# Performance work log

Hardware: AMD Instinct MI355X
Metric: run time of the kernel (lower is better)

The kernel has to match this reference:

```python
import jax, jax.numpy as jnp
import numpy as np

B, L, D, T = 32, 512, 1024, 256
MAX_MENTION_LEN = 10
NEG_INF = float('-inf')


def _static_bounds_and_keep():
    # Full (start, end) grid, flattened row-major like torch's .view(-1, 2)
    s = np.repeat(np.arange(L), L)
    e = np.tile(np.arange(L), L)
    bounds = np.stack([s, e], axis=-1)            # [L*L, 2]
    keep = (e - s) <= MAX_MENTION_LEN             # static per-position mask
    idx = np.nonzero(keep)[0]
    return jnp.asarray(bounds[keep], jnp.int32), jnp.asarray(idx, jnp.int32)


def setup_inputs() -> dict:
    key = jax.random.key(0)
    k0, k1, k2 = jax.random.split(key, 3)
    text_encodings = jax.random.normal(k0, (B, L, D), dtype=jnp.float32)
    mask_ctxt = jnp.ones((B, L), dtype=jnp.int32)
    # word -> wordpiece mapping: [start, end_exclusive); values kept in [1, L)
    tokens_mapping = jax.random.randint(k1, (B, T, 2), 1, L).astype(jnp.int32)
    W = jax.random.normal(k2, (D, 3), dtype=jnp.float32) * 0.02
    b = jnp.zeros((3,), dtype=jnp.float32)
    return {"text_encodings": text_encodings, "mask_ctxt": mask_ctxt,
            "tokens_mapping": tokens_mapping, "W": W, "b": b}


def reference(text_encodings, mask_ctxt, tokens_mapping, W, b):
    # per-token start / end / mention logits
    logits = jnp.einsum('bld,dk->blk', text_encodings, W) + b  # [B, L, 3]
    valid_tok = (mask_ctxt == 1)
    start_lp = jnp.where(valid_tok, logits[:, :, 0], NEG_INF)
    end_lp = jnp.where(valid_tok, logits[:, :, 1], NEG_INF)
    mention_lp = jnp.where(valid_tok, logits[:, :, 2], NEG_INF)

    # scores[b, s, e] = start[b, s] + end[b, e] + sum_{i=s..e} mention[b, i]
    scores = start_lp[:, :, None] + end_lp[:, None, :]          # [B, L, L]
    csum = jnp.cumsum(mention_lp, axis=1)                        # [B, L]
    csum_prev = jnp.concatenate(
        [jnp.zeros((csum.shape[0], 1), csum.dtype), csum[:, :-1]], axis=1)
    scores = scores + (csum[:, None, :] - csum_prev[:, :, None])

    # mention_sizes > 0  <=>  e >= s
    pos = jnp.arange(L)
    size_ok = pos[None, :, None] <= pos[None, None, :]           # [1, L, L]

    # token-boundary masks (scatter 1 at word starts / ends, zero col 0)
    bidx = jnp.arange(tokens_mapping.shape[0])[:, None]
    ts = jnp.zeros(mask_ctxt.shape, jnp.int32).at[bidx, tokens_mapping[:, :, 0]].set(1)
    ts = ts.at[:, 0].set(0)
    te = jnp.zeros(mask_ctxt.shape, jnp.int32).at[bidx, tokens_mapping[:, :, 1] - 1].set(1)
    te = te.at[:, 0].set(0)
    vse = ts[:, :, None] * te[:, None, :]                        # bmm outer product

    valid = size_ok & (mask_ctxt[:, :, None] > 0) & (vse > 0)
    scores = jnp.where(valid, scores, NEG_INF)

    scores_flat = scores.reshape(scores.shape[0], -1)            # [B, L*L]
    bounds_keep, keep_idx = _static_bounds_and_keep()
    out_scores = scores_flat[:, keep_idx]                        # [B, K]
    out_bounds = jnp.broadcast_to(bounds_keep[None],
                                  (scores.shape[0],) + bounds_keep.shape)
    return out_scores, out_bounds
```

## Files before the change

kernel.cpp:

```cpp
#include <hip/hip_runtime.h>
#include <math.h>

#define BB 32
#define LL 512
#define DD 1024
#define TT 256
#define NK 136393
#define NK_LIN 131273
#define S_LIN 502
#define NEG_BIG  -3.0e38f
#define NEG_MASK -1.0e30f
#define P_TOT (BB * NK)
#define SC4 (P_TOT / 4)
#define GEMV_BLOCKS 4096
#define MEMSET_BLOCKS ((SC4 + 255) / 256)
#define BCHUNKS ((NK + 255) / 256)
#define BGROUPS 2
#define BOUNDS_BLOCKS (BCHUNKS * BGROUPS)
#define PERIOD 9
#define QMAX 1066
#define MEGA_BLOCKS (PERIOD * QMAX)

typedef float f4v __attribute__((ext_vector_type(4)));
typedef float f2v __attribute__((ext_vector_type(2)));

__device__ __forceinline__ int off_s(int s) {
    return (s <= S_LIN) ? s * (s + 21) / 2 : NK_LIN + (s - S_LIN) * LL;
}

__global__ __launch_bounds__(256) void mega_kernel(
    const float* __restrict__ text, const float* __restrict__ W,
    const float* __restrict__ bias, const int* __restrict__ mask,
    float* __restrict__ out,
    float* __restrict__ slp, float* __restrict__ elp, float* __restrict__ mlp)
{
    const int id = blockIdx.x;
    const int q  = id / PERIOD;
    const int r  = id - q * PERIOD;

    if (r < 4) {
        const int g = q * 4 + r;
        if (g >= GEMV_BLOCKS) return;
        const int wid  = threadIdx.x >> 6;
        const int lane = threadIdx.x & 63;
        const int row  = g * 4 + wid;
        const f4v* t4 = (const f4v*)(text + (size_t)row * DD);
        const f4v* w4 = (const f4v*)W;
        float a0 = 0.f, a1 = 0.f, a2 = 0.f;
#pragma unroll
        for (int j = 0; j < 4; ++j) {
            const int fi = lane + j * 64;
            f4v v  = t4[fi];
            f4v w0 = w4[fi * 3 + 0];
            f4v w1 = w4[fi * 3 + 1];
            f4v w2 = w4[fi * 3 + 2];
            a0 += v.x * w0.x;  a1 += v.x * w0.y;  a2 += v.x * w0.z;
            a0 += v.y * w0.w;  a1 += v.y * w1.x;  a2 += v.y * w1.y;
            a0 += v.z * w1.z;  a1 += v.z * w1.w;  a2 += v.z * w2.x;
            a0 += v.w * w2.y;  a1 += v.w * w2.z;  a2 += v.w * w2.w;
        }
#pragma unroll
        for (int o = 32; o; o >>= 1) {
            a0 += __shfl_down(a0, o);
            a1 += __shfl_down(a1, o);
            a2 += __shfl_down(a2, o);
        }
        if (lane == 0) {
            const int m = mask[row];
            slp[row] = (m == 1) ? a0 + bias[0] : NEG_MASK;
            elp[row] = (m == 1) ? a1 + bias[1] : NEG_MASK;
            mlp[row] = (m == 1) ? a2 + bias[2] : NEG_MASK;
        }
        return;
    }

    if (r < 8) {
        const int m = q * 4 + (r - 4);
        if (m >= MEMSET_BLOCKS) return;
        const int i = m * 256 + threadIdx.x;
        if (i < SC4) {
            f4v neg = {NEG_BIG, NEG_BIG, NEG_BIG, NEG_BIG};
            ((f4v*)out)[i] = neg;
        }
        return;
    }

    if (q >= BOUNDS_BLOCKS) return;
    const int c = q % BCHUNKS;
    const int g = q / BCHUNKS;
    const int p = c * 256 + threadIdx.x;
    if (p >= NK) return;
    int s, e;
    if (p >= NK_LIN) {
        const int rr = p - NK_LIN;
        s = S_LIN + (rr >> 9);
        e = rr & 511;
    } else {
        float f = sqrtf(8.0f * (float)p + 441.0f);
        s = (int)((f - 21.0f) * 0.5f);
        if (s < 0) s = 0;
        if (s > 501) s = 501;
        while ((s + 1) * (s + 22) / 2 <= p) ++s;
        while (s * (s + 21) / 2 > p) --s;
        e = p - s * (s + 21) / 2;
    }
    f2v v = {(float)s, (float)e};
    f2v* bp = (f2v*)(out + (size_t)P_TOT);
#pragma unroll
    for (int j = 0; j < 16; ++j) {
        const int b = g * 16 + j;
        bp[(size_t)b * NK + p] = v;
    }
}

__global__ __launch_bounds__(512) void scatter_kernel(
    const float* __restrict__ slp, const float* __restrict__ elp,
    const float* __restrict__ mlp, const int* __restrict__ mask,
    const int* __restrict__ tmap, float* __restrict__ out)
{
    const int b = blockIdx.x;
    const int t = threadIdx.x;
    __shared__ float sl[LL], el[LL], ml[LL];
    __shared__ unsigned char tsl[LL], tel[LL];

    tsl[t] = 0; tel[t] = 0;
    const int idx = b * LL + t;
    sl[t] = slp[idx]; el[t] = elp[idx]; ml[t] = mlp[idx];
    __syncthreads();
    if (t < TT) {
        int s0 = tmap[((size_t)b * TT + t) * 2 + 0];
        int e0 = tmap[((size_t)b * TT + t) * 2 + 1] - 1;
        s0 = min(max(s0, 0), LL - 1);
        e0 = min(max(e0, 0), LL - 1);
        tsl[s0] = 1;
        tel[e0] = 1;
    }
    __syncthreads();

    const int s = t;
    if (s > 0 && tsl[s] && mask[idx] == 1) {
        const size_t obase = (size_t)b * NK + off_s(s);
        const float sv = sl[s];
        const int emax = min(LL - 1, s + 10);
        float w = 0.f;
        for (int e = s; e <= emax; ++e) {
            w += ml[e];
            if (tel[e]) {
                float sc = sv + el[e] + w;
                if (sc < -1.0e29f) sc = NEG_BIG;
                out[obase + e] = sc;
            }
        }
    }
}

extern "C" void kernel_launch(void* const* d_in, const int* in_sizes, int n_in,
                              void* d_out, int out_size, void* d_ws, size_t ws_size,
                              hipStream_t stream) {
    const float* text = (const float*)d_in[0];
    const int*   mask = (const int*)d_in[1];
    const int*   tmap = (const int*)d_in[2];
    const float* W    = (const float*)d_in[3];
    const float* bias = (const float*)d_in[4];
    float* out = (float*)d_out;

    float* slp = (float*)d_ws;
    float* elp = slp + (size_t)BB * LL;
    float* mlp = elp + (size_t)BB * LL;

    mega_kernel<<<MEGA_BLOCKS, 256, 0, stream>>>(text, W, bias, mask, out,
                                                 slp, elp, mlp);
    scatter_kernel<<<BB, 512, 0, stream>>>(slp, elp, mlp, mask, tmap, out);
}
```

Baseline: 28.53 us.

## Split fused mega kernel into separate fill, GEMV and parallel scatter kernels

Replaces the single interleaved mega kernel with a write kernel (fill and bounds), a separate GEMV kernel, and a scatter kernel launched over a 2D grid so each block handles one span length. Splitting the scatter across 11 times more blocks spreads the per-batch tail work over more CUs. The cost is an extra kernel launch, redundant shared-memory setup in every tail block, and the loss of the overlap between GEMV and memset that the interleaved block schedule provided.

```diff
diff --git a/kernel.cpp b/kernel.cpp
--- a/kernel.cpp
+++ b/kernel.cpp
@@ -12,14 +12,10 @@
 #define NEG_MASK -1.0e30f
 #define P_TOT (BB * NK)
 #define SC4 (P_TOT / 4)
-#define GEMV_BLOCKS 4096
 #define MEMSET_BLOCKS ((SC4 + 255) / 256)
 #define BCHUNKS ((NK + 255) / 256)
-#define BGROUPS 2
-#define BOUNDS_BLOCKS (BCHUNKS * BGROUPS)
-#define PERIOD 9
-#define QMAX 1066
-#define MEGA_BLOCKS (PERIOD * QMAX)
+#define D1_BLOCKS (MEMSET_BLOCKS + 2 * BCHUNKS)
+#define GEMV_BLOCKS (BB * LL / 4)
 
 typedef float f4v __attribute__((ext_vector_type(4)));
 typedef float f2v __attribute__((ext_vector_type(2)));
@@ -28,56 +24,13 @@
     return (s <= S_LIN) ? s * (s + 21) / 2 : NK_LIN + (s - S_LIN) * LL;
 }
 
-__global__ __launch_bounds__(256) void mega_kernel(
-    const float* __restrict__ text, const float* __restrict__ W,
-    const float* __restrict__ bias, const int* __restrict__ mask,
-    float* __restrict__ out,
-    float* __restrict__ slp, float* __restrict__ elp, float* __restrict__ mlp)
+__global__ __launch_bounds__(256) void write_kernel(float* __restrict__ out)
 {
     const int id = blockIdx.x;
-    const int q  = id / PERIOD;
-    const int r  = id - q * PERIOD;
+    const int t  = threadIdx.x;
 
-    if (r < 4) {
-        const int g = q * 4 + r;
-        if (g >= GEMV_BLOCKS) return;
-        const int wid  = threadIdx.x >> 6;
-        const int lane = threadIdx.x & 63;
-        const int row  = g * 4 + wid;
-        const f4v* t4 = (const f4v*)(text + (size_t)row * DD);
-        const f4v* w4 = (const f4v*)W;
-        float a0 = 0.f, a1 = 0.f, a2 = 0.f;
-#pragma unroll
-        for (int j = 0; j < 4; ++j) {
-            const int fi = lane + j * 64;
-            f4v v  = t4[fi];
-            f4v w0 = w4[fi * 3 + 0];
-            f4v w1 = w4[fi * 3 + 1];
-            f4v w2 = w4[fi * 3 + 2];
-            a0 += v.x * w0.x;  a1 += v.x * w0.y;  a2 += v.x * w0.z;
-            a0 += v.y * w0.w;  a1 += v.y * w1.x;  a2 += v.y * w1.y;
-            a0 += v.z * w1.z;  a1 += v.z * w1.w;  a2 += v.z * w2.x;
-            a0 += v.w * w2.y;  a1 += v.w * w2.z;  a2 += v.w * w2.w;
-        }
-#pragma unroll
-        for (int o = 32; o; o >>= 1) {
-            a0 += __shfl_down(a0, o);
-            a1 += __shfl_down(a1, o);
-            a2 += __shfl_down(a2, o);
-        }
-        if (lane == 0) {
-            const int m = mask[row];
-            slp[row] = (m == 1) ? a0 + bias[0] : NEG_MASK;
-            elp[row] = (m == 1) ? a1 + bias[1] : NEG_MASK;
-            mlp[row] = (m == 1) ? a2 + bias[2] : NEG_MASK;
-        }
-        return;
-    }
-
-    if (r < 8) {
-        const int m = q * 4 + (r - 4);
-        if (m >= MEMSET_BLOCKS) return;
-        const int i = m * 256 + threadIdx.x;
+    if (id < MEMSET_BLOCKS) {
+        const int i = id * 256 + t;
         if (i < SC4) {
             f4v neg = {NEG_BIG, NEG_BIG, NEG_BIG, NEG_BIG};
             ((f4v*)out)[i] = neg;
@@ -85,10 +38,10 @@
         return;
     }
 
-    if (q >= BOUNDS_BLOCKS) return;
-    const int c = q % BCHUNKS;
-    const int g = q / BCHUNKS;
-    const int p = c * 256 + threadIdx.x;
+    const int q = id - MEMSET_BLOCKS;
+    const int g = (q >= BCHUNKS) ? 1 : 0;
+    const int c = q - g * BCHUNKS;
+    const int p = c * 256 + t;
     if (p >= NK) return;
     int s, e;
     if (p >= NK_LIN) {
@@ -113,18 +66,56 @@
     }
 }
 
-__global__ __launch_bounds__(512) void scatter_kernel(
+__global__ __launch_bounds__(256) void gemv_kernel(
+    const float* __restrict__ text, const float* __restrict__ W,
+    const float* __restrict__ bias, const int* __restrict__ mask,
+    float* __restrict__ slp, float* __restrict__ elp, float* __restrict__ mlp)
+{
+    const int wid  = threadIdx.x >> 6;
+    const int lane = threadIdx.x & 63;
+    const int row  = blockIdx.x * 4 + wid;
+    const f4v* t4 = (const f4v*)(text + (size_t)row * DD);
+    const f4v* w4 = (const f4v*)W;
+    float a0 = 0.f, a1 = 0.f, a2 = 0.f;
+#pragma unroll
+    for (int j = 0; j < 4; ++j) {
+        const int fi = lane + j * 64;
+        f4v v  = t4[fi];
+        f4v w0 = w4[fi * 3 + 0];
+        f4v w1 = w4[fi * 3 + 1];
+        f4v w2 = w4[fi * 3 + 2];
+        a0 += v.x * w0.x;  a1 += v.x * w0.y;  a2 += v.x * w0.z;
+        a0 += v.y * w0.w;  a1 += v.y * w1.x;  a2 += v.y * w1.y;
+        a0 += v.z * w1.z;  a1 += v.z * w1.w;  a2 += v.z * w2.x;
+        a0 += v.w * w2.y;  a1 += v.w * w2.z;  a2 += v.w * w2.w;
+    }
+#pragma unroll
+    for (int o = 32; o; o >>= 1) {
+        a0 += __shfl_down(a0, o);
+        a1 += __shfl_down(a1, o);
+        a2 += __shfl_down(a2, o);
+    }
+    if (lane == 0) {
+        const int m = mask[row];
+        slp[row] = (m == 1) ? a0 + bias[0] : NEG_MASK;
+        elp[row] = (m == 1) ? a1 + bias[1] : NEG_MASK;
+        mlp[row] = (m == 1) ? a2 + bias[2] : NEG_MASK;
+    }
+}
+
+__global__ __launch_bounds__(512) void tail_kernel(
     const float* __restrict__ slp, const float* __restrict__ elp,
     const float* __restrict__ mlp, const int* __restrict__ mask,
     const int* __restrict__ tmap, float* __restrict__ out)
 {
     const int b = blockIdx.x;
+    const int j = blockIdx.y;
     const int t = threadIdx.x;
     __shared__ float sl[LL], el[LL], ml[LL];
     __shared__ unsigned char tsl[LL], tel[LL];
 
+    const int idx = b * LL + t;
     tsl[t] = 0; tel[t] = 0;
-    const int idx = b * LL + t;
     sl[t] = slp[idx]; el[t] = elp[idx]; ml[t] = mlp[idx];
     __syncthreads();
     if (t < TT) {
@@ -138,19 +129,13 @@
     __syncthreads();
 
     const int s = t;
-    if (s > 0 && tsl[s] && mask[idx] == 1) {
-        const size_t obase = (size_t)b * NK + off_s(s);
-        const float sv = sl[s];
-        const int emax = min(LL - 1, s + 10);
+    const int e = s + j;
+    if (s > 0 && e < LL && tsl[s] && tel[e] && mask[idx] == 1) {
         float w = 0.f;
-        for (int e = s; e <= emax; ++e) {
-            w += ml[e];
-            if (tel[e]) {
-                float sc = sv + el[e] + w;
-                if (sc < -1.0e29f) sc = NEG_BIG;
-                out[obase + e] = sc;
-            }
-        }
+        for (int l = s; l <= e; ++l) w += ml[l];
+        float sc = sl[s] + el[e] + w;
+        if (sc < -1.0e29f) sc = NEG_BIG;
+        out[(size_t)b * NK + off_s(s) + e] = sc;
     }
 }
 
@@ -168,7 +153,9 @@
     float* elp = slp + (size_t)BB * LL;
     float* mlp = elp + (size_t)BB * LL;
 
-    mega_kernel<<<MEGA_BLOCKS, 256, 0, stream>>>(text, W, bias, mask, out,
+    write_kernel<<<D1_BLOCKS, 256, 0, stream>>>(out);
+    gemv_kernel<<<GEMV_BLOCKS, 256, 0, stream>>>(text, W, bias, mask,
                                                  slp, elp, mlp);
-    scatter_kernel<<<BB, 512, 0, stream>>>(slp, elp, mlp, mask, tmap, out);
+    dim3 g3(BB, 11);
+    tail_kernel<<<g3, 512, 0, stream>>>(slp, elp, mlp, mask, tmap, out);
 }
```

New measurement: 28.70 us. Within noise of the previous version (+0.6%).
